# Performance work log

Hardware: AMD Instinct MI355X
Metric: run time of the kernel (lower is better)

The kernel has to match this reference:

```python
import jax, jax.numpy as jnp
import numpy as np


def setup_inputs() -> dict:
    key = jax.random.key(0)
    k1, k2 = jax.random.split(key)
    B, T, D = 32, 1024, 384
    encodings = jax.random.normal(k1, (B, T, D), dtype=jnp.float32)
    durations = jax.random.randint(k2, (B, T), 0, 8, dtype=jnp.int32)
    return {"encodings": encodings, "durations": durations}


def reference(encodings, durations):
    # encodings: [B, T, D] float; durations: [B, T] int (torch code rounds .item())
    B, T, D = encodings.shape
    reps = jnp.round(durations).astype(jnp.int32)            # [B, T]
    csum = jnp.cumsum(reps, axis=1)                          # [B, T] exclusive end offsets
    totals = csum[:, -1]                                     # [B] expanded length per batch
    # max_len computed from concrete durations (dynamic output length, like the torch code)
    max_len = int(jnp.max(totals))
    pos = jnp.arange(max_len)                                # [L]
    # frame p belongs to token j where csum[j-1] <= p < csum[j] -> searchsorted right
    idx = jax.vmap(lambda c: jnp.searchsorted(c, pos, side="right"))(csum)  # [B, L]
    idx = jnp.minimum(idx, T - 1)
    out = jnp.take_along_axis(encodings, idx[:, :, None], axis=1)           # [B, L, D]
    mask = pos[None, :] < totals[:, None]                                   # [B, L]
    return jnp.where(mask[:, :, None], out, jnp.zeros((), dtype=encodings.dtype))
```

## Files before the change

### kernel.cpp

```cpp
#include <hip/hip_runtime.h>

#define NB 32
#define NT 1024
#define ND 384
#define ND4 (ND / 4)

__global__ void scan_kernel(const int* __restrict__ dur, int* __restrict__ csum) {
    __shared__ int s[NT];
    const int b = blockIdx.x;
    const int t = threadIdx.x;
    s[t] = dur[b * NT + t];
    __syncthreads();
    #pragma unroll
    for (int off = 1; off < NT; off <<= 1) {
        int add = (t >= off) ? s[t - off] : 0;
        __syncthreads();
        s[t] += add;
        __syncthreads();
    }
    csum[b * NT + t] = s[t];
}

__global__ void __launch_bounds__(256)
gather_kernel(const float4* __restrict__ enc,
              const int* __restrict__ csum,
              float4* __restrict__ out,
              int max_len, int f4_per_batch) {
    __shared__ int sc[NT];
    const int b = blockIdx.y;
    for (int i = threadIdx.x; i < NT; i += blockDim.x)
        sc[i] = csum[b * NT + i];
    __syncthreads();
    const int total = sc[NT - 1];

    const size_t enc_base = (size_t)b * NT * ND4;
    const size_t out_base = (size_t)b * max_len * ND4;
    const int stride = gridDim.x * blockDim.x;

    for (int j = blockIdx.x * blockDim.x + threadIdx.x; j < f4_per_batch; j += stride) {
        const int p  = j / ND4;
        const int d4 = j - p * ND4;
        float4 val;
        if (p < total) {
            int lo = 0, hi = NT - 1;
            while (lo < hi) {
                int mid = (lo + hi) >> 1;
                if (sc[mid] <= p) lo = mid + 1; else hi = mid;
            }
            val = enc[enc_base + (size_t)lo * ND4 + d4];
        } else {
            val = make_float4(0.f, 0.f, 0.f, 0.f);
        }
        out[out_base + j] = val;
    }
}

extern "C" void kernel_launch(void* const* d_in, const int* in_sizes, int n_in,
                              void* d_out, int out_size, void* d_ws, size_t ws_size,
                              hipStream_t stream) {
    const float* enc = (const float*)d_in[0];
    const int*   dur = (const int*)d_in[1];
    float* out = (float*)d_out;

    const int max_len = out_size / (NB * ND);
    int* csum = (int*)d_ws;

    scan_kernel<<<NB, NT, 0, stream>>>(dur, csum);

    const int f4pb = max_len * ND4;
    dim3 grid(64, NB);
    gather_kernel<<<grid, 256, 0, stream>>>(
        (const float4*)enc, csum, (float4*)out, max_len, f4pb);
}
```

Before: 229.1 us.

## Scatter per-frame token indices in scan kernel, replacing per-element binary search

```diff
diff --git a/kernel.cpp b/kernel.cpp
--- a/kernel.cpp
+++ b/kernel.cpp
@@ -5,11 +5,16 @@
 #define ND 384
 #define ND4 (ND / 4)
 
-__global__ void scan_kernel(const int* __restrict__ dur, int* __restrict__ csum) {
+__global__ void __launch_bounds__(NT)
+scan_scatter_kernel(const int* __restrict__ dur,
+                    int* __restrict__ idx,
+                    int* __restrict__ totals,
+                    int max_len) {
     __shared__ int s[NT];
     const int b = blockIdx.x;
     const int t = threadIdx.x;
-    s[t] = dur[b * NT + t];
+    const int d = dur[b * NT + t];
+    s[t] = d;
     __syncthreads();
     #pragma unroll
     for (int off = 1; off < NT; off <<= 1) {
@@ -18,38 +23,34 @@
         s[t] += add;
         __syncthreads();
     }
-    csum[b * NT + t] = s[t];
+    const int csum_t = s[t];
+    int* idx_b = idx + (size_t)b * max_len;
+    for (int p = csum_t - d; p < csum_t; ++p)
+        idx_b[p] = t;
+    if (t == NT - 1)
+        totals[b] = csum_t;
 }
 
 __global__ void __launch_bounds__(256)
 gather_kernel(const float4* __restrict__ enc,
-              const int* __restrict__ csum,
+              const int* __restrict__ idx,
+              const int* __restrict__ totals,
               float4* __restrict__ out,
               int max_len, int f4_per_batch) {
-    __shared__ int sc[NT];
     const int b = blockIdx.y;
-    for (int i = threadIdx.x; i < NT; i += blockDim.x)
-        sc[i] = csum[b * NT + i];
-    __syncthreads();
-    const int total = sc[NT - 1];
-
+    const int total_f4 = totals[b] * ND4;
+    const int* idx_b = idx + (size_t)b * max_len;
     const size_t enc_base = (size_t)b * NT * ND4;
-    const size_t out_base = (size_t)b * max_len * ND4;
+    const size_t out_base = (size_t)b * (size_t)max_len * ND4;
     const int stride = gridDim.x * blockDim.x;
 
     for (int j = blockIdx.x * blockDim.x + threadIdx.x; j < f4_per_batch; j += stride) {
-        const int p  = j / ND4;
-        const int d4 = j - p * ND4;
-        float4 val;
-        if (p < total) {
-            int lo = 0, hi = NT - 1;
-            while (lo < hi) {
-                int mid = (lo + hi) >> 1;
-                if (sc[mid] <= p) lo = mid + 1; else hi = mid;
-            }
-            val = enc[enc_base + (size_t)lo * ND4 + d4];
-        } else {
-            val = make_float4(0.f, 0.f, 0.f, 0.f);
+        float4 val = make_float4(0.f, 0.f, 0.f, 0.f);
+        if (j < total_f4) {
+            const int p  = j / ND4;
+            const int d4 = j - p * ND4;
+            const int t  = idx_b[p];
+            val = enc[enc_base + (size_t)t * ND4 + d4];
         }
         out[out_base + j] = val;
     }
@@ -63,12 +64,15 @@
     float* out = (float*)d_out;
 
     const int max_len = out_size / (NB * ND);
-    int* csum = (int*)d_ws;
 
-    scan_kernel<<<NB, NT, 0, stream>>>(dur, csum);
+    int* totals = (int*)d_ws;
+    int* idx    = totals + NB;
+
+    scan_scatter_kernel<<<NB, NT, 0, stream>>>(dur, idx, totals, max_len);
 
     const int f4pb = max_len * ND4;
-    dim3 grid(64, NB);
+    const int blocks_x = (f4pb + 1023) / 1024;
+    dim3 grid(blocks_x, NB);
     gather_kernel<<<grid, 256, 0, stream>>>(
-        (const float4*)enc, csum, (float4*)out, max_len, f4pb);
+        (const float4*)enc, idx, totals, (float4*)out, max_len, f4pb);
 }
```

New measurement: 233.1 us. No clear change (+1.8%).
